# Kernel tuning notes

Measured on AMD Instinct MI355X. Metric: run time of the kernel, lower is better.

## Reference

```python
import math
import jax, jax.numpy as jnp
import numpy as np

D_MODEL = 256
N_HEAD = 8
D_HEAD = D_MODEL // N_HEAD
GROUP = 8  # window side
SCALE = D_HEAD ** (-0.5)


def _window_partition(x):
    # x: [B, N, C] with N = hw*hw, hw divisible by GROUP
    B, N, C = x.shape
    hw = int(math.isqrt(N))
    ng = hw // GROUP                      # windows per side
    gs = GROUP * GROUP                    # tokens per window
    x = x.reshape(B, ng, GROUP, ng, GROUP, C)
    x = x.transpose(0, 1, 3, 2, 4, 5)     # [B, ng, ng, g, g, C]
    x = x.reshape(B, ng * ng, gs, N_HEAD, D_HEAD)
    return x.transpose(0, 1, 3, 2, 4)     # [B, nw, H, gs, d]


def _window_merge(x, B, N, C):
    # x: [B, nw, H, gs, d] -> [B, N, C]
    hw = int(math.isqrt(N))
    ng = hw // GROUP
    gs = GROUP * GROUP
    x = x.transpose(0, 1, 3, 2, 4)        # [B, nw, gs, H, d]
    x = x.reshape(B, ng, ng, GROUP, GROUP, C)
    x = x.transpose(0, 1, 3, 2, 4, 5)     # [B, ng, g, ng, g, C]
    return x.reshape(B, N, C)


def setup_inputs() -> dict:
    key = jax.random.key(0)
    kq, kk, kv, kw = jax.random.split(key, 4)
    B, N, C = 8, 16384, D_MODEL
    q = jax.random.normal(kq, (B, N, C), dtype=jnp.float32)
    k = jax.random.normal(kk, (B, N, C), dtype=jnp.float32)
    v = jax.random.normal(kv, (B, N, C), dtype=jnp.float32)
    W_fc = jax.random.normal(kw, (C, C), dtype=jnp.float32) * 0.02  # nn.Linear weight [out, in]
    return {"q": q, "k": k, "v": v, "W_fc": W_fc}


def reference(q, k, v, W_fc):
    B, N, C = q.shape
    qw = _window_partition(q)   # [B, nw, H, gs, d]
    kw_ = _window_partition(k)
    vw = _window_partition(v)
    attn = jnp.einsum('bwhqd,bwhkd->bwhqk', qw, kw_) * SCALE
    attn = jax.nn.softmax(attn, axis=-1)
    out = jnp.einsum('bwhqk,bwhkd->bwhqd', attn, vw)
    out = _window_merge(out, B, N, C)      # [B, N, C]
    return out @ W_fc.T
```

## Files before the change

### kernel.cpp

```cpp
#include <hip/hip_runtime.h>
#include <hip/hip_bf16.h>


typedef __attribute__((ext_vector_type(8))) short bf8;
typedef __attribute__((ext_vector_type(4))) float f4;

#define SCALE 0.17677669529663687f
#define CC (SCALE * 1.4426950408889634f)

static __device__ __forceinline__ unsigned cvtpk(float lo, float hi) {
  unsigned r;
  asm("v_cvt_pk_bf16_f32 %0, %1, %2" : "=v"(r) : "v"(lo), "v"(hi));
  return r;
}
union FragU { unsigned u[4]; bf8 v; };

static __device__ __forceinline__ bf8 load_bf8_cvt(const float* __restrict__ p) {
  float4 a = *(const float4*)p;
  float4 b = *(const float4*)(p + 4);
  FragU f;
  f.u[0] = cvtpk(a.x, a.y);
  f.u[1] = cvtpk(a.z, a.w);
  f.u[2] = cvtpk(b.x, b.y);
  f.u[3] = cvtpk(b.z, b.w);
  return f.v;
}
static __device__ __forceinline__ bf8 load_bf8_cvt_scaled(const float* __restrict__ p) {
  float4 a = *(const float4*)p;
  float4 b = *(const float4*)(p + 4);
  FragU f;
  f.u[0] = cvtpk(a.x * CC, a.y * CC);
  f.u[1] = cvtpk(a.z * CC, a.w * CC);
  f.u[2] = cvtpk(b.x * CC, b.y * CC);
  f.u[3] = cvtpk(b.z * CC, b.w * CC);
  return f.v;
}

__global__ void wcvt(const float* __restrict__ W, unsigned short* __restrict__ Wb) {
  const int i = (blockIdx.x * 256 + threadIdx.x) * 4;
  float4 w = *(const float4*)(W + i);
  unsigned u01 = cvtpk(w.x, w.y);
  unsigned u23 = cvtpk(w.z, w.w);
  uint2 o;
  o.x = u01; o.y = u23;
  *(uint2*)(Wb + i) = o;
}

template <bool WB16>
__global__ __launch_bounds__(256, 4) void win_attn_fc(
    const float* __restrict__ q, const float* __restrict__ k,
    const float* __restrict__ v, const void* __restrict__ Wp,
    float* __restrict__ out) {
  __shared__ unsigned short smem[18432];
  const int tid  = threadIdx.x;
  const int wave = tid >> 6;
  const int lane = tid & 63;
  const int g    = lane >> 4;
  const int c16  = lane & 15;

  const int blk = blockIdx.x;
  const int b   = blk >> 8;
  const int wy  = (blk >> 4) & 15;
  const int wx  = blk & 15;
  const long tokbase = (long)b * 16384 + (long)(wy * 8) * 128 + wx * 8;

  unsigned short* VT0 = smem + wave * 4608;
  unsigned short* VT1 = VT0 + 2304;

  unsigned opk[2][2][4][2];

  const int  srcA = c16 + ((g & 1) << 5);
  const bool hi   = (g >> 1) != 0;
  const int v_tcol = lane >> 3;
  const int v_cg   = lane & 7;

  #pragma unroll
  for (int hh = 0; hh < 2; ++hh) {
    const int h = wave * 2 + hh;
    unsigned short* VTh = hh ? VT1 : VT0;
    #pragma unroll
    for (int i = 0; i < 8; ++i) {
      const long r = tokbase + i * 128 + v_tcol;
      float4 vv = *(const float4*)(v + r * 256 + h * 32 + v_cg * 4);
      unsigned u01 = cvtpk(vv.x, vv.y);
      unsigned u23 = cvtpk(vv.z, vv.w);
      const int tswz = 8 * (i ^ v_cg) + v_tcol;
      VTh[(4*v_cg + 0) * 72 + tswz] = (unsigned short)u01;
      VTh[(4*v_cg + 1) * 72 + tswz] = (unsigned short)(u01 >> 16);
      VTh[(4*v_cg + 2) * 72 + tswz] = (unsigned short)u23;
      VTh[(4*v_cg + 3) * 72 + tswz] = (unsigned short)(u23 >> 16);
    }
  }

  bf8 qf[2][4], kf[2][4];
  #pragma unroll
  for (int hh = 0; hh < 2; ++hh) {
    const int h = wave * 2 + hh;
    #pragma unroll
    for (int t = 0; t < 4; ++t) {
      const int m = 16 * t + c16;
      const long r = tokbase + (m >> 3) * 128 + (m & 7);
      kf[hh][t] = load_bf8_cvt(k + r * 256 + h * 32 + g * 8);
      qf[hh][t] = load_bf8_cvt_scaled(q + r * 256 + h * 32 + g * 8);
    }
  }

  #pragma unroll
  for (int hh = 0; hh < 2; ++hh) {
    unsigned short* VTh = hh ? VT1 : VT0;
    #pragma unroll
    for (int ti = 0; ti < 4; ++ti) {
      f4 st[4];
      __builtin_amdgcn_s_setprio(1);
      #pragma unroll
      for (int tj = 0; tj < 4; ++tj) {
        f4 z = {0.f, 0.f, 0.f, 0.f};
        st[tj] = __builtin_amdgcn_mfma_f32_16x16x32_bf16(kf[hh][tj], qf[hh][ti], z, 0, 0, 0);
      }
      __builtin_amdgcn_s_setprio(0);
      float ds = 0.f;
      unsigned PW[4][2];
      #pragma unroll
      for (int tj = 0; tj < 4; ++tj) {
        float p0 = exp2f(st[tj][0]);
        float p1 = exp2f(st[tj][1]);
        float p2 = exp2f(st[tj][2]);
        float p3 = exp2f(st[tj][3]);
        ds += (p0 + p1) + (p2 + p3);
        PW[tj][0] = cvtpk(p0, p1);
        PW[tj][1] = cvtpk(p2, p3);
      }
      ds += __shfl_xor(ds, 16);
      ds += __shfl_xor(ds, 32);
      const float rc = __builtin_amdgcn_rcpf(ds);
      f4 acc0 = {0.f, 0.f, 0.f, 0.f};
      f4 acc1 = {0.f, 0.f, 0.f, 0.f};
      #pragma unroll
      for (int kt = 0; kt < 2; ++kt) {
        unsigned a0 = __shfl(PW[2*kt  ][0], srcA);
        unsigned a1 = __shfl(PW[2*kt  ][1], srcA);
        unsigned a2 = __shfl(PW[2*kt  ][0], srcA + 16);
        unsigned a3 = __shfl(PW[2*kt  ][1], srcA + 16);
        unsigned b0 = __shfl(PW[2*kt+1][0], srcA);
        unsigned b1 = __shfl(PW[2*kt+1][1], srcA);
        unsigned b2 = __shfl(PW[2*kt+1][0], srcA + 16);
        unsigned b3 = __shfl(PW[2*kt+1][1], srcA + 16);
        FragU pf;
        pf.u[0] = hi ? b0 : a0;
        pf.u[1] = hi ? b1 : a1;
        pf.u[2] = hi ? b2 : a2;
        pf.u[3] = hi ? b3 : a3;
        bf8 vf0 = *(const bf8*)(VTh + (c16     ) * 72 + 8 * ((4*kt + g) ^ (c16 >> 2)));
        bf8 vf1 = *(const bf8*)(VTh + (16 + c16) * 72 + 8 * ((4*kt + g) ^ (4 + (c16 >> 2))));
        __builtin_amdgcn_s_setprio(1);
        acc0 = __builtin_amdgcn_mfma_f32_16x16x32_bf16(vf0, pf.v, acc0, 0, 0, 0);
        acc1 = __builtin_amdgcn_mfma_f32_16x16x32_bf16(vf1, pf.v, acc1, 0, 0, 0);
        __builtin_amdgcn_s_setprio(0);
      }
      opk[hh][0][ti][0] = cvtpk(acc0[0] * rc, acc0[1] * rc);
      opk[hh][0][ti][1] = cvtpk(acc0[2] * rc, acc0[3] * rc);
      opk[hh][1][ti][0] = cvtpk(acc1[0] * rc, acc1[1] * rc);
      opk[hh][1][ti][1] = cvtpk(acc1[2] * rc, acc1[3] * rc);
    }
  }

  __syncthreads();
  unsigned short* inter = smem;
  #pragma unroll
  for (int hh = 0; hh < 2; ++hh)
    #pragma unroll
    for (int dt = 0; dt < 2; ++dt)
      #pragma unroll
      for (int ti = 0; ti < 4; ++ti) {
        const int addr = (16*ti + c16) * 280 + (wave*2 + hh) * 32 + 16*dt + 4*g;
        uint2 wv;
        wv.x = opk[hh][dt][ti][0];
        wv.y = opk[hh][dt][ti][1];
        *(uint2*)(inter + addr) = wv;
      }
  __syncthreads();

  f4 acc[4][4];
  #pragma unroll
  for (int mt = 0; mt < 4; ++mt)
    #pragma unroll
    for (int nt = 0; nt < 4; ++nt) {
      f4 z = {0.f, 0.f, 0.f, 0.f};
      acc[mt][nt] = z;
    }
  const float* Wf          = (const float*)Wp;
  const unsigned short* Wb = (const unsigned short*)Wp;
  #pragma unroll
  for (int ks = 0; ks < 8; ++ks) {
    bf8 af[4], wf[4];
    #pragma unroll
    for (int mt = 0; mt < 4; ++mt)
      af[mt] = *(const bf8*)(inter + (16*mt + c16) * 280 + 32*ks + 8*g);
    #pragma unroll
    for (int nt = 0; nt < 4; ++nt) {
      const long widx = (long)(64*wave + 16*nt + c16) * 256 + 32*ks + 8*g;
      if (WB16) wf[nt] = *(const bf8*)(Wb + widx);
      else      wf[nt] = load_bf8_cvt(Wf + widx);
    }
    __builtin_amdgcn_s_setprio(1);
    #pragma unroll
    for (int mt = 0; mt < 4; ++mt)
      #pragma unroll
      for (int nt = 0; nt < 4; ++nt)
        acc[mt][nt] = __builtin_amdgcn_mfma_f32_16x16x32_bf16(af[mt], wf[nt], acc[mt][nt], 0, 0, 0);
    __builtin_amdgcn_s_setprio(0);
  }

  #pragma unroll
  for (int mt = 0; mt < 4; ++mt) {
    #pragma unroll
    for (int r = 0; r < 4; ++r) {
      const int m = 16*mt + 4*g + r;
      const long row = tokbase + (m >> 3) * 128 + (m & 7);
      float* op = out + row * 256 + 64*wave + c16;
      #pragma unroll
      for (int nt = 0; nt < 4; ++nt)
        op[16*nt] = acc[mt][nt][r];
    }
  }
}

extern "C" void kernel_launch(void* const* d_in, const int* in_sizes, int n_in,
                              void* d_out, int out_size, void* d_ws, size_t ws_size,
                              hipStream_t stream) {
  const float* q = (const float*)d_in[0];
  const float* k = (const float*)d_in[1];
  const float* v = (const float*)d_in[2];
  const float* W = (const float*)d_in[3];
  float* out = (float*)d_out;
  const int B = in_sizes[0] / (16384 * 256);
  const size_t wbytes = 65536 * sizeof(unsigned short);
  if (ws_size >= wbytes) {
    wcvt<<<dim3(64), dim3(256), 0, stream>>>(W, (unsigned short*)d_ws);
    win_attn_fc<true><<<dim3(B * 256), dim3(256), 0, stream>>>(q, k, v, d_ws, out);
  } else {
    win_attn_fc<false><<<dim3(B * 256), dim3(256), 0, stream>>>(q, k, v, W, out);
  }
}
```

Baseline: 127.5 us.

## Process two windows per block and prefetch second window during first

Each block now handles two adjacent 8x8 windows. The V staging and Q/K loads for the second window are issued in the middle of the first window's attention compute, so global-load latency can overlap with the MFMA work. The intermediate LDS layout drops its row padding in favour of an XOR swizzle, and LDS grows to 64KB. Launch bounds drop to 2 blocks per CU and the grid is halved, which reduces occupancy and raises register pressure in exchange for the overlap.

```diff
diff --git a/kernel.cpp b/kernel.cpp
--- a/kernel.cpp
+++ b/kernel.cpp
@@ -39,188 +39,207 @@
 __global__ void wcvt(const float* __restrict__ W, unsigned short* __restrict__ Wb) {
   const int i = (blockIdx.x * 256 + threadIdx.x) * 4;
   float4 w = *(const float4*)(W + i);
-  unsigned u01 = cvtpk(w.x, w.y);
-  unsigned u23 = cvtpk(w.z, w.w);
   uint2 o;
-  o.x = u01; o.y = u23;
+  o.x = cvtpk(w.x, w.y);
+  o.y = cvtpk(w.z, w.w);
   *(uint2*)(Wb + i) = o;
 }
 
 template <bool WB16>
-__global__ __launch_bounds__(256, 4) void win_attn_fc(
+__global__ __launch_bounds__(256, 2) void win_attn_fc(
     const float* __restrict__ q, const float* __restrict__ k,
     const float* __restrict__ v, const void* __restrict__ Wp,
     float* __restrict__ out) {
-  __shared__ unsigned short smem[18432];
+  __shared__ unsigned short smem[32768];
   const int tid  = threadIdx.x;
   const int wave = tid >> 6;
   const int lane = tid & 63;
   const int g    = lane >> 4;
   const int c16  = lane & 15;
 
-  const int blk = blockIdx.x;
-  const int b   = blk >> 8;
-  const int wy  = (blk >> 4) & 15;
-  const int wx  = blk & 15;
-  const long tokbase = (long)b * 16384 + (long)(wy * 8) * 128 + wx * 8;
-
-  unsigned short* VT0 = smem + wave * 4608;
-  unsigned short* VT1 = VT0 + 2304;
-
-  unsigned opk[2][2][4][2];
+  const int wi0 = blockIdx.x * 2;
+  const int b   = wi0 >> 8;
+  const int wy  = (wi0 >> 4) & 15;
+  const int wx  = wi0 & 15;
+  const long tb0 = (long)b * 16384 + (long)(wy * 8) * 128 + wx * 8;
+  const long tb1 = tb0 + 8;
 
   const int  srcA = c16 + ((g & 1) << 5);
   const bool hi   = (g >> 1) != 0;
   const int v_tcol = lane >> 3;
   const int v_cg   = lane & 7;
-
-  #pragma unroll
-  for (int hh = 0; hh < 2; ++hh) {
-    const int h = wave * 2 + hh;
-    unsigned short* VTh = hh ? VT1 : VT0;
-    #pragma unroll
-    for (int i = 0; i < 8; ++i) {
-      const long r = tokbase + i * 128 + v_tcol;
-      float4 vv = *(const float4*)(v + r * 256 + h * 32 + v_cg * 4);
-      unsigned u01 = cvtpk(vv.x, vv.y);
-      unsigned u23 = cvtpk(vv.z, vv.w);
-      const int tswz = 8 * (i ^ v_cg) + v_tcol;
-      VTh[(4*v_cg + 0) * 72 + tswz] = (unsigned short)u01;
-      VTh[(4*v_cg + 1) * 72 + tswz] = (unsigned short)(u01 >> 16);
-      VTh[(4*v_cg + 2) * 72 + tswz] = (unsigned short)u23;
-      VTh[(4*v_cg + 3) * 72 + tswz] = (unsigned short)(u23 >> 16);
-    }
-  }
+  const int rx4    = (c16 & 7) << 2;
 
   bf8 qf[2][4], kf[2][4];
-  #pragma unroll
-  for (int hh = 0; hh < 2; ++hh) {
-    const int h = wave * 2 + hh;
-    #pragma unroll
-    for (int t = 0; t < 4; ++t) {
-      const int m = 16 * t + c16;
-      const long r = tokbase + (m >> 3) * 128 + (m & 7);
-      kf[hh][t] = load_bf8_cvt(k + r * 256 + h * 32 + g * 8);
-      qf[hh][t] = load_bf8_cvt_scaled(q + r * 256 + h * 32 + g * 8);
-    }
-  }
-
-  #pragma unroll
-  for (int hh = 0; hh < 2; ++hh) {
-    unsigned short* VTh = hh ? VT1 : VT0;
-    #pragma unroll
-    for (int ti = 0; ti < 4; ++ti) {
-      f4 st[4];
-      __builtin_amdgcn_s_setprio(1);
-      #pragma unroll
-      for (int tj = 0; tj < 4; ++tj) {
-        f4 z = {0.f, 0.f, 0.f, 0.f};
-        st[tj] = __builtin_amdgcn_mfma_f32_16x16x32_bf16(kf[hh][tj], qf[hh][ti], z, 0, 0, 0);
-      }
-      __builtin_amdgcn_s_setprio(0);
-      float ds = 0.f;
-      unsigned PW[4][2];
-      #pragma unroll
-      for (int tj = 0; tj < 4; ++tj) {
-        float p0 = exp2f(st[tj][0]);
-        float p1 = exp2f(st[tj][1]);
-        float p2 = exp2f(st[tj][2]);
-        float p3 = exp2f(st[tj][3]);
-        ds += (p0 + p1) + (p2 + p3);
-        PW[tj][0] = cvtpk(p0, p1);
-        PW[tj][1] = cvtpk(p2, p3);
-      }
-      ds += __shfl_xor(ds, 16);
-      ds += __shfl_xor(ds, 32);
-      const float rc = __builtin_amdgcn_rcpf(ds);
-      f4 acc0 = {0.f, 0.f, 0.f, 0.f};
-      f4 acc1 = {0.f, 0.f, 0.f, 0.f};
-      #pragma unroll
-      for (int kt = 0; kt < 2; ++kt) {
-        unsigned a0 = __shfl(PW[2*kt  ][0], srcA);
-        unsigned a1 = __shfl(PW[2*kt  ][1], srcA);
-        unsigned a2 = __shfl(PW[2*kt  ][0], srcA + 16);
-        unsigned a3 = __shfl(PW[2*kt  ][1], srcA + 16);
-        unsigned b0 = __shfl(PW[2*kt+1][0], srcA);
-        unsigned b1 = __shfl(PW[2*kt+1][1], srcA);
-        unsigned b2 = __shfl(PW[2*kt+1][0], srcA + 16);
-        unsigned b3 = __shfl(PW[2*kt+1][1], srcA + 16);
-        FragU pf;
-        pf.u[0] = hi ? b0 : a0;
-        pf.u[1] = hi ? b1 : a1;
-        pf.u[2] = hi ? b2 : a2;
-        pf.u[3] = hi ? b3 : a3;
-        bf8 vf0 = *(const bf8*)(VTh + (c16     ) * 72 + 8 * ((4*kt + g) ^ (c16 >> 2)));
-        bf8 vf1 = *(const bf8*)(VTh + (16 + c16) * 72 + 8 * ((4*kt + g) ^ (4 + (c16 >> 2))));
-        __builtin_amdgcn_s_setprio(1);
-        acc0 = __builtin_amdgcn_mfma_f32_16x16x32_bf16(vf0, pf.v, acc0, 0, 0, 0);
-        acc1 = __builtin_amdgcn_mfma_f32_16x16x32_bf16(vf1, pf.v, acc1, 0, 0, 0);
-        __builtin_amdgcn_s_setprio(0);
-      }
-      opk[hh][0][ti][0] = cvtpk(acc0[0] * rc, acc0[1] * rc);
-      opk[hh][0][ti][1] = cvtpk(acc0[2] * rc, acc0[3] * rc);
-      opk[hh][1][ti][0] = cvtpk(acc1[0] * rc, acc1[1] * rc);
-      opk[hh][1][ti][1] = cvtpk(acc1[2] * rc, acc1[3] * rc);
-    }
-  }
-
-  __syncthreads();
-  unsigned short* inter = smem;
-  #pragma unroll
-  for (int hh = 0; hh < 2; ++hh)
-    #pragma unroll
-    for (int dt = 0; dt < 2; ++dt)
-      #pragma unroll
-      for (int ti = 0; ti < 4; ++ti) {
-        const int addr = (16*ti + c16) * 280 + (wave*2 + hh) * 32 + 16*dt + 4*g;
-        uint2 wv;
-        wv.x = opk[hh][dt][ti][0];
-        wv.y = opk[hh][dt][ti][1];
-        *(uint2*)(inter + addr) = wv;
-      }
-  __syncthreads();
-
-  f4 acc[4][4];
-  #pragma unroll
-  for (int mt = 0; mt < 4; ++mt)
-    #pragma unroll
-    for (int nt = 0; nt < 4; ++nt) {
-      f4 z = {0.f, 0.f, 0.f, 0.f};
-      acc[mt][nt] = z;
-    }
+
+  auto stage_V = [&](int wsel, long tb) {
+    #pragma unroll
+    for (int hh = 0; hh < 2; ++hh) {
+      const int h = wave * 2 + hh;
+      unsigned short* VTh = smem + wsel * 16384 + wave * 4096 + hh * 2048;
+      #pragma unroll
+      for (int i = 0; i < 8; ++i) {
+        const long r = tb + i * 128 + v_tcol;
+        float4 vv = *(const float4*)(v + r * 256 + h * 32 + v_cg * 4);
+        unsigned u01 = cvtpk(vv.x, vv.y);
+        unsigned u23 = cvtpk(vv.z, vv.w);
+        const int tswz = 8 * (i ^ v_cg) + v_tcol;
+        VTh[(4*v_cg + 0) * 64 + tswz] = (unsigned short)u01;
+        VTh[(4*v_cg + 1) * 64 + tswz] = (unsigned short)(u01 >> 16);
+        VTh[(4*v_cg + 2) * 64 + tswz] = (unsigned short)u23;
+        VTh[(4*v_cg + 3) * 64 + tswz] = (unsigned short)(u23 >> 16);
+      }
+    }
+  };
+  auto load_QK = [&](long tb) {
+    #pragma unroll
+    for (int hh = 0; hh < 2; ++hh) {
+      const int h = wave * 2 + hh;
+      #pragma unroll
+      for (int t = 0; t < 4; ++t) {
+        const int m = 16 * t + c16;
+        const long r = tb + (m >> 3) * 128 + (m & 7);
+        kf[hh][t] = load_bf8_cvt(k + r * 256 + h * 32 + g * 8);
+        qf[hh][t] = load_bf8_cvt_scaled(q + r * 256 + h * 32 + g * 8);
+      }
+    }
+  };
+
+  stage_V(0, tb0);
+  load_QK(tb0);
+
   const float* Wf          = (const float*)Wp;
   const unsigned short* Wb = (const unsigned short*)Wp;
+
   #pragma unroll
-  for (int ks = 0; ks < 8; ++ks) {
-    bf8 af[4], wf[4];
+  for (int wsel = 0; wsel < 2; ++wsel) {
+    const long tb = wsel ? tb1 : tb0;
+    unsigned opk[2][2][4][2];
+
+    #pragma unroll
+    for (int hh = 0; hh < 2; ++hh) {
+      unsigned short* VTh = smem + wsel * 16384 + wave * 4096 + hh * 2048;
+      #pragma unroll
+      for (int ti = 0; ti < 4; ++ti) {
+        f4 st[4];
+        __builtin_amdgcn_s_setprio(1);
+        #pragma unroll
+        for (int tj = 0; tj < 4; ++tj) {
+          f4 z = {0.f, 0.f, 0.f, 0.f};
+          st[tj] = __builtin_amdgcn_mfma_f32_16x16x32_bf16(kf[hh][tj], qf[hh][ti], z, 0, 0, 0);
+        }
+        __builtin_amdgcn_s_setprio(0);
+        float ds = 0.f;
+        unsigned PW[4][2];
+        #pragma unroll
+        for (int tj = 0; tj < 4; ++tj) {
+          float p0 = exp2f(st[tj][0]);
+          float p1 = exp2f(st[tj][1]);
+          float p2 = exp2f(st[tj][2]);
+          float p3 = exp2f(st[tj][3]);
+          ds += (p0 + p1) + (p2 + p3);
+          PW[tj][0] = cvtpk(p0, p1);
+          PW[tj][1] = cvtpk(p2, p3);
+        }
+        ds += __shfl_xor(ds, 16);
+        ds += __shfl_xor(ds, 32);
+        const float rc = __builtin_amdgcn_rcpf(ds);
+
+        if (wsel == 0 && hh == 1 && ti == 3) {
+          stage_V(1, tb1);
+          load_QK(tb1);
+        }
+
+        f4 acc0 = {0.f, 0.f, 0.f, 0.f};
+        f4 acc1 = {0.f, 0.f, 0.f, 0.f};
+        #pragma unroll
+        for (int kt = 0; kt < 2; ++kt) {
+          unsigned x0 = __shfl(PW[2*kt  ][0], srcA);
+          unsigned x1 = __shfl(PW[2*kt  ][1], srcA);
+          unsigned x2 = __shfl(PW[2*kt  ][0], srcA + 16);
+          unsigned x3 = __shfl(PW[2*kt  ][1], srcA + 16);
+          unsigned y0 = __shfl(PW[2*kt+1][0], srcA);
+          unsigned y1 = __shfl(PW[2*kt+1][1], srcA);
+          unsigned y2 = __shfl(PW[2*kt+1][0], srcA + 16);
+          unsigned y3 = __shfl(PW[2*kt+1][1], srcA + 16);
+          FragU pf;
+          pf.u[0] = hi ? y0 : x0;
+          pf.u[1] = hi ? y1 : x1;
+          pf.u[2] = hi ? y2 : x2;
+          pf.u[3] = hi ? y3 : x3;
+          bf8 vf0 = *(const bf8*)(VTh + (c16     ) * 64 + 8 * ((4*kt + g) ^ (c16 >> 2)));
+          bf8 vf1 = *(const bf8*)(VTh + (16 + c16) * 64 + 8 * ((4*kt + g) ^ (4 + (c16 >> 2))));
+          __builtin_amdgcn_s_setprio(1);
+          acc0 = __builtin_amdgcn_mfma_f32_16x16x32_bf16(vf0, pf.v, acc0, 0, 0, 0);
+          acc1 = __builtin_amdgcn_mfma_f32_16x16x32_bf16(vf1, pf.v, acc1, 0, 0, 0);
+          __builtin_amdgcn_s_setprio(0);
+        }
+        opk[hh][0][ti][0] = cvtpk(acc0[0] * rc, acc0[1] * rc);
+        opk[hh][0][ti][1] = cvtpk(acc0[2] * rc, acc0[3] * rc);
+        opk[hh][1][ti][0] = cvtpk(acc1[0] * rc, acc1[1] * rc);
+        opk[hh][1][ti][1] = cvtpk(acc1[2] * rc, acc1[3] * rc);
+      }
+    }
+
+    __syncthreads();
+    unsigned short* inter = smem + wsel * 16384;
+    #pragma unroll
+    for (int hh = 0; hh < 2; ++hh)
+      #pragma unroll
+      for (int dt = 0; dt < 2; ++dt)
+        #pragma unroll
+        for (int ti = 0; ti < 4; ++ti) {
+          const int T    = 16*ti + c16;
+          const int blkc = ((wave*2 + hh)*4 + 2*dt + (g >> 1)) ^ rx4;
+          uint2 wv;
+          wv.x = opk[hh][dt][ti][0];
+          wv.y = opk[hh][dt][ti][1];
+          *(uint2*)(inter + T * 256 + blkc * 8 + 4*(g & 1)) = wv;
+        }
+    __syncthreads();
+
+    f4 acc[4][4];
     #pragma unroll
     for (int mt = 0; mt < 4; ++mt)
-      af[mt] = *(const bf8*)(inter + (16*mt + c16) * 280 + 32*ks + 8*g);
-    #pragma unroll
-    for (int nt = 0; nt < 4; ++nt) {
-      const long widx = (long)(64*wave + 16*nt + c16) * 256 + 32*ks + 8*g;
-      if (WB16) wf[nt] = *(const bf8*)(Wb + widx);
-      else      wf[nt] = load_bf8_cvt(Wf + widx);
-    }
-    __builtin_amdgcn_s_setprio(1);
-    #pragma unroll
-    for (int mt = 0; mt < 4; ++mt)
-      #pragma unroll
-      for (int nt = 0; nt < 4; ++nt)
-        acc[mt][nt] = __builtin_amdgcn_mfma_f32_16x16x32_bf16(af[mt], wf[nt], acc[mt][nt], 0, 0, 0);
-    __builtin_amdgcn_s_setprio(0);
-  }
-
-  #pragma unroll
-  for (int mt = 0; mt < 4; ++mt) {
-    #pragma unroll
-    for (int r = 0; r < 4; ++r) {
-      const int m = 16*mt + 4*g + r;
-      const long row = tokbase + (m >> 3) * 128 + (m & 7);
-      float* op = out + row * 256 + 64*wave + c16;
-      #pragma unroll
-      for (int nt = 0; nt < 4; ++nt)
-        op[16*nt] = acc[mt][nt][r];
+      #pragma unroll
+      for (int nt = 0; nt < 4; ++nt) {
+        f4 z = {0.f, 0.f, 0.f, 0.f};
+        acc[mt][nt] = z;
+      }
+    #pragma unroll
+    for (int ks = 0; ks < 8; ++ks) {
+      bf8 af[4], wf[4];
+      #pragma unroll
+      for (int mt = 0; mt < 4; ++mt) {
+        const int T = 16*mt + c16;
+        af[mt] = *(const bf8*)(inter + T * 256 + ((4*ks + g) ^ rx4) * 8);
+      }
+      #pragma unroll
+      for (int nt = 0; nt < 4; ++nt) {
+        const long widx = (long)(64*wave + 16*nt + c16) * 256 + 32*ks + 8*g;
+        if (WB16) wf[nt] = *(const bf8*)(Wb + widx);
+        else      wf[nt] = load_bf8_cvt(Wf + widx);
+      }
+      __builtin_amdgcn_s_setprio(1);
+      #pragma unroll
+      for (int mt = 0; mt < 4; ++mt)
+        #pragma unroll
+        for (int nt = 0; nt < 4; ++nt)
+          acc[mt][nt] = __builtin_amdgcn_mfma_f32_16x16x32_bf16(af[mt], wf[nt], acc[mt][nt], 0, 0, 0);
+      __builtin_amdgcn_s_setprio(0);
+    }
+
+    #pragma unroll
+    for (int mt = 0; mt < 4; ++mt) {
+      #pragma unroll
+      for (int r = 0; r < 4; ++r) {
+        const int m = 16*mt + 4*g + r;
+        const long row = tb + (m >> 3) * 128 + (m & 7);
+        float* op = out + row * 256 + 64*wave + c16;
+        #pragma unroll
+        for (int nt = 0; nt < 4; ++nt)
+          op[16*nt] = acc[mt][nt][r];
+      }
     }
   }
 }
@@ -237,8 +256,8 @@
   const size_t wbytes = 65536 * sizeof(unsigned short);
   if (ws_size >= wbytes) {
     wcvt<<<dim3(64), dim3(256), 0, stream>>>(W, (unsigned short*)d_ws);
-    win_attn_fc<true><<<dim3(B * 256), dim3(256), 0, stream>>>(q, k, v, d_ws, out);
+    win_attn_fc<true><<<dim3(B * 128), dim3(256), 0, stream>>>(q, k, v, d_ws, out);
   } else {
-    win_attn_fc<false><<<dim3(B * 256), dim3(256), 0, stream>>>(q, k, v, W, out);
+    win_attn_fc<false><<<dim3(B * 128), dim3(256), 0, stream>>>(q, k, v, W, out);
   }
 }
```

New measurement: 140.7 us. 10.3% more time.
